# Kernel tuning notes

Hardware: AMD Instinct MI355X
Metric: run time of the kernel (lower is better)

Reference implementation:

```python
import jax, jax.numpy as jnp
import numpy as np

N, D, E = 100000, 32, 1600000
EH, NH = 32, 16
TAU = 0.1


def setup_inputs() -> dict:
    key = jax.random.key(0)
    ks = jax.random.split(key, 12)
    x = jax.random.normal(ks[0], (N, D), dtype=jnp.float32)
    edge_index = jax.random.randint(ks[1], (2, E), 0, N, dtype=jnp.int32)
    hsd = jax.random.normal(ks[2], (N,), dtype=jnp.float32)
    s_e1 = 1.0 / np.sqrt(D + 2)
    s_e2 = 1.0 / np.sqrt(EH)
    s_n2 = 1.0 / np.sqrt(NH)
    We1 = jax.random.uniform(ks[3], (D + 2, EH), jnp.float32, -s_e1, s_e1)
    be1 = jax.random.uniform(ks[4], (EH,), jnp.float32, -s_e1, s_e1)
    We2 = jax.random.uniform(ks[5], (EH, 1), jnp.float32, -s_e2, s_e2)
    be2 = jax.random.uniform(ks[6], (1,), jnp.float32, -s_e2, s_e2)
    Wn1 = jax.random.uniform(ks[7], (1, NH), jnp.float32, -1.0, 1.0)
    bn1 = jax.random.uniform(ks[8], (NH,), jnp.float32, -1.0, 1.0)
    Wn2 = jax.random.uniform(ks[9], (NH, 1), jnp.float32, -s_n2, s_n2)
    bn2 = jax.random.uniform(ks[10], (1,), jnp.float32, -s_n2, s_n2)
    return {"x": x, "hsd": hsd, "We1": We1, "be1": be1, "We2": We2, "be2": be2,
            "Wn1": Wn1, "bn1": bn1, "Wn2": Wn2, "bn2": bn2, "edge_index": edge_index}


def reference(x, hsd, We1, be1, We2, be2, Wn1, bn1, Wn2, bn2, edge_index):
    row, col = edge_index[0], edge_index[1]
    n = x.shape[0]
    # normalized HSD (torch.std is unbiased, ddof=1)
    hsd_norm = (hsd - hsd.mean()) / (jnp.std(hsd, ddof=1) + 1e-8)
    # edge MLP input: [hsd_u, hsd_v, |x_u - x_v|]  -> (E, D+2)
    diff_abs = jnp.abs(x[row] - x[col])
    edge_in = jnp.concatenate([hsd_norm[row][:, None], hsd_norm[col][:, None], diff_abs], axis=1)
    h = jax.nn.relu(edge_in @ We1 + be1)
    e_uv = (h @ We2 + be2)[:, 0]  # (E,)
    # segment softmax over destination (col)
    logits = e_uv / TAU
    seg_max = jax.ops.segment_max(logits, col, num_segments=n)
    seg_max = jnp.where(jnp.isfinite(seg_max), seg_max, 0.0)
    ex = jnp.exp(logits - seg_max[col])
    denom = jax.ops.segment_sum(ex, col, num_segments=n)
    alpha_uv = (ex / (denom[col] + 1e-16))[:, None]  # (E,1)
    # node-level gate
    gh = jax.nn.relu(hsd_norm[:, None] @ Wn1 + bn1)
    alpha_bar = jax.nn.sigmoid(gh @ Wn2 + bn2)  # (N,1)
    # degree normalization
    ones = jnp.ones(row.shape[0], dtype=x.dtype)
    src_deg = jnp.sqrt(jnp.clip(jax.ops.segment_sum(ones, row, num_segments=n), 1.0))
    dst_deg = jnp.sqrt(jnp.clip(jax.ops.segment_sum(ones, col, num_segments=n), 1.0))
    edge_w = 1.0 / (src_deg[row] * dst_deg[col])
    low_pass = jax.ops.segment_sum(edge_w[:, None] * x[row], col, num_segments=n)
    high_pass = jax.ops.segment_sum(alpha_uv * (x[col] - x[row]), col, num_segments=n)
    return (1.0 - alpha_bar) * low_pass + alpha_bar * high_pass
```

## Files before the change

### kernel.cpp

```cpp
#include <hip/hip_runtime.h>

#define D_FEAT 32
#define IN_DIM 34
#define EHID 32
#define NHID 16
#define INV_TAU 10.0f
#define SCAN_CHUNK 1024
#define EPB 256
#define XS 36
#define TILE 8192
#define CAP 7680

__global__ __launch_bounds__(256) void k1_hsd_stats(const float* __restrict__ hsd,
                                                    double* __restrict__ stats, int N) {
    double s = 0.0, s2 = 0.0;
    for (int i = blockIdx.x * 256 + threadIdx.x; i < N; i += gridDim.x * 256) {
        double v = (double)hsd[i];
        s += v; s2 += v * v;
    }
    for (int off = 32; off > 0; off >>= 1) {
        s  += __shfl_down(s,  off, 64);
        s2 += __shfl_down(s2, off, 64);
    }
    __shared__ double ls[4], ls2[4];
    int wid = threadIdx.x >> 6, lid = threadIdx.x & 63;
    if (lid == 0) { ls[wid] = s; ls2[wid] = s2; }
    __syncthreads();
    if (threadIdx.x == 0) {
        double ts = 0.0, t2 = 0.0;
        for (int w = 0; w < 4; ++w) { ts += ls[w]; t2 += ls2[w]; }
        atomicAdd(stats, ts);
        atomicAdd(stats + 1, t2);
    }
}

__global__ __launch_bounds__(256) void k2_node_prep(const float* __restrict__ hsd,
                                                    const double* __restrict__ stats,
                                                    const float* __restrict__ Wn1,
                                                    const float* __restrict__ bn1,
                                                    const float* __restrict__ Wn2,
                                                    const float* __restrict__ bn2,
                                                    float* __restrict__ hsd_norm,
                                                    float* __restrict__ alpha_bar, int N) {
    int n = blockIdx.x * 256 + threadIdx.x;
    if (n >= N) return;
    double sum = stats[0], sumsq = stats[1];
    double mean = sum / (double)N;
    double var  = (sumsq - sum * sum / (double)N) / (double)(N - 1);
    float stdv  = (float)sqrt(var);
    float hn = (hsd[n] - (float)mean) / (stdv + 1e-8f);
    hsd_norm[n] = hn;
    float acc = bn2[0];
#pragma unroll
    for (int k = 0; k < NHID; ++k)
        acc += fmaxf(fmaf(hn, Wn1[k], bn1[k]), 0.0f) * Wn2[k];
    alpha_bar[n] = 1.0f / (1.0f + __expf(-acc));
}

__global__ __launch_bounds__(256) void s1_hist(const int* __restrict__ ei,
                                               int* __restrict__ histV,
                                               int* __restrict__ histU,
                                               int E, int NB, int T) {
    __shared__ int hv[512], hu[512];
    int t = threadIdx.x;
    for (int b = t; b < 512; b += 256) { hv[b] = 0; hu[b] = 0; }
    __syncthreads();
    int base = blockIdx.x * TILE;
    for (int i = t; i < TILE; i += 256) {
        int e = base + i;
        if (e < E) {
            int u = ei[e], v = ei[E + e];
            atomicAdd(&hv[v >> 8], 1);
            atomicAdd(&hu[u >> 8], 1);
        }
    }
    __syncthreads();
    for (int b = t; b < NB; b += 256) {
        histV[b * T + blockIdx.x] = hv[b];
        histU[b * T + blockIdx.x] = hu[b];
    }
}

__global__ __launch_bounds__(256) void scan_k1(const int* __restrict__ cnt,
                                               int* __restrict__ out,
                                               int* __restrict__ partials, int N) {
    __shared__ int lds[256];
    int base = blockIdx.x * SCAN_CHUNK;
    int t = threadIdx.x;
    int v[4]; int loc = 0;
#pragma unroll
    for (int k = 0; k < 4; ++k) {
        int idx = base + t * 4 + k;
        v[k] = (idx < N) ? cnt[idx] : 0;
        loc += v[k];
    }
    lds[t] = loc; __syncthreads();
    for (int off = 1; off < 256; off <<= 1) {
        int a = (t >= off) ? lds[t - off] : 0;
        __syncthreads();
        lds[t] += a;
        __syncthreads();
    }
    int run = (t > 0) ? lds[t - 1] : 0;
    if (t == 255) partials[blockIdx.x] = lds[255];
#pragma unroll
    for (int k = 0; k < 4; ++k) {
        run += v[k];
        int idx = base + t * 4 + k;
        if (idx < N) out[idx + 1] = run;
    }
    if (blockIdx.x == 0 && t == 0) out[0] = 0;
}

__global__ __launch_bounds__(256) void scan_k2(int* __restrict__ partials, int B) {
    __shared__ int lds[256];
    int t = threadIdx.x;
    lds[t] = (t < B) ? partials[t] : 0;
    __syncthreads();
    for (int off = 1; off < 256; off <<= 1) {
        int a = (t >= off) ? lds[t - off] : 0;
        __syncthreads();
        lds[t] += a;
        __syncthreads();
    }
    if (t < B) partials[t] = (t > 0) ? lds[t - 1] : 0;
}

__global__ __launch_bounds__(256) void scan_k3(int* __restrict__ out,
                                               const int* __restrict__ partials, int N) {
    int i = blockIdx.x * 256 + threadIdx.x;
    if (i >= N) return;
    out[i + 1] += partials[i / SCAN_CHUNK];
}

__global__ __launch_bounds__(256) void s2_scatter(const int* __restrict__ ei,
                                                  const int* __restrict__ scanV,
                                                  const int* __restrict__ scanU,
                                                  int2* __restrict__ coarse,
                                                  int* __restrict__ coarseU,
                                                  int E, int NB, int T) {
    __shared__ int curV[512], curU[512];
    int t = threadIdx.x;
    for (int b = t; b < NB; b += 256) {
        curV[b] = scanV[b * T + blockIdx.x];
        curU[b] = scanU[b * T + blockIdx.x];
    }
    __syncthreads();
    int base = blockIdx.x * TILE;
    for (int i = t; i < TILE; i += 256) {
        int e = base + i;
        if (e < E) {
            int u = ei[e], v = ei[E + e];
            int pv = atomicAdd(&curV[v >> 8], 1);
            coarse[pv] = make_int2(u, v);
            int pu = atomicAdd(&curU[u >> 8], 1);
            coarseU[pu] = u;
        }
    }
}

__global__ __launch_bounds__(256) void s3_binsort(int2* __restrict__ coarse,
                                                  const int* __restrict__ scanV,
                                                  int* __restrict__ dst_off,
                                                  int E, int N, int NB, int T) {
    __shared__ int2 buf[CAP];
    __shared__ int cnt[256];
    __shared__ int cur[256];
    int t = threadIdx.x;
    int bin = blockIdx.x;
    int start = scanV[bin * T];
    int endv  = scanV[(bin + 1) * T];
    int n = endv - start;
    if (n > CAP) n = CAP;

    for (int i = t; i < n; i += 256) buf[i] = coarse[start + i];
    cnt[t] = 0;
    __syncthreads();
    for (int i = t; i < n; i += 256) atomicAdd(&cnt[buf[i].y & 255], 1);
    __syncthreads();
    for (int off = 1; off < 256; off <<= 1) {
        int a = (t >= off) ? cnt[t - off] : 0;
        __syncthreads();
        cnt[t] += a;
        __syncthreads();
    }
    int mybase = (t > 0) ? cnt[t - 1] : 0;
    int vglob = (bin << 8) + t;
    if (vglob < N) dst_off[vglob] = start + mybase;
    if (bin == 0 && t == 0) dst_off[N] = E;
    cur[t] = mybase;
    __syncthreads();
    for (int i = t; i < n; i += 256) {
        int lv = buf[i].y & 255;
        int p = atomicAdd(&cur[lv], 1);
        coarse[start + p] = buf[i];
    }
}

__global__ __launch_bounds__(256) void s3b_srccnt(const int* __restrict__ coarseU,
                                                  const int* __restrict__ scanU,
                                                  int* __restrict__ src_cnt,
                                                  int N, int NB, int T) {
    __shared__ int cnt[256];
    int t = threadIdx.x;
    int bin = blockIdx.x;
    int start = scanU[bin * T];
    int endv  = scanU[(bin + 1) * T];
    cnt[t] = 0;
    __syncthreads();
    for (int i = start + t; i < endv; i += 256) atomicAdd(&cnt[coarseU[i] & 255], 1);
    __syncthreads();
    int vglob = (bin << 8) + t;
    if (vglob < N) src_cnt[vglob] = cnt[t];
}

__global__ __launch_bounds__(256) void k3c_mlp(const float* __restrict__ x,
                                               const float* __restrict__ hsd_norm,
                                               const float* __restrict__ We1,
                                               const float* __restrict__ be1,
                                               const float* __restrict__ We2,
                                               const float* __restrict__ be2,
                                               const int2* __restrict__ esorted,
                                               float* __restrict__ logit_sorted, int E) {
    __shared__ float sxu[EPB * XS];
    int t = threadIdx.x;
    int base = blockIdx.x * EPB;

    int q = t & 7;
#pragma unroll
    for (int k = 0; k < 8; ++k) {
        int s = (t >> 3) + 32 * k;
        int e = base + s;
        int u = esorted[(e < E) ? e : (E - 1)].x;
        float4 val = *(const float4*)(x + (size_t)u * D_FEAT + 4 * q);
        *(float4*)(sxu + s * XS + 4 * q) = val;
    }
    __syncthreads();

    int e = base + t;
    if (e >= E) return;
    int2 uv = esorted[e];
    int u = uv.x, v = uv.y;

    float in0 = hsd_norm[u];
    float in1 = hsd_norm[v];

    float diff[D_FEAT];
    const float4* xv = (const float4*)(x + (size_t)v * D_FEAT);
#pragma unroll
    for (int qq = 0; qq < 8; ++qq) {
        float4 a = *(const float4*)(sxu + t * XS + 4 * qq);
        float4 b = xv[qq];
        diff[4 * qq + 0] = fabsf(a.x - b.x);
        diff[4 * qq + 1] = fabsf(a.y - b.y);
        diff[4 * qq + 2] = fabsf(a.z - b.z);
        diff[4 * qq + 3] = fabsf(a.w - b.w);
    }

    float h[EHID];
#pragma unroll
    for (int j = 0; j < EHID; ++j)
        h[j] = fmaf(in0, We1[j], fmaf(in1, We1[EHID + j], be1[j]));
#pragma unroll
    for (int i = 0; i < D_FEAT; ++i) {
        float a = diff[i];
#pragma unroll
        for (int j = 0; j < EHID; ++j)
            h[j] = fmaf(a, We1[(i + 2) * EHID + j], h[j]);
    }
    float acc = be2[0];
#pragma unroll
    for (int j = 0; j < EHID; ++j)
        acc += fmaxf(h[j], 0.0f) * We2[j];

    logit_sorted[e] = acc * INV_TAU;
}

__global__ __launch_bounds__(256) void k5_gather(const float* __restrict__ x,
                                                 const int* __restrict__ dst_off,
                                                 const int2* __restrict__ esorted,
                                                 const float* __restrict__ logit_sorted,
                                                 const int* __restrict__ src_cnt,
                                                 const float* __restrict__ alpha_bar,
                                                 float* __restrict__ out, int N) {
    int wid = threadIdx.x >> 6;
    int lane = threadIdx.x & 63;
    int v = blockIdx.x * 4 + wid;
    if (v >= N) return;

    int beg = dst_off[v], end = dst_off[v + 1];

    float m = -INFINITY;
    for (int t = beg + lane; t < end; t += 64) m = fmaxf(m, logit_sorted[t]);
#pragma unroll
    for (int off = 1; off < 64; off <<= 1) m = fmaxf(m, __shfl_xor(m, off, 64));
    float s = 0.0f;
    for (int t = beg + lane; t < end; t += 64) s += __expf(logit_sorted[t] - m);
#pragma unroll
    for (int off = 1; off < 64; off <<= 1) s += __shfl_xor(s, off, 64);
    float denom = s;
    float inv_denom = 1.0f / (denom + 1e-16f);

    float ab = alpha_bar[v];
    float one_ab = 1.0f - ab;
    float inv_sdv = rsqrtf(fmaxf((float)(end - beg), 1.0f));
    int half = lane >> 5;
    int d = lane & 31;

    float acc = 0.0f;
    int jj = beg + half;
    for (; jj + 2 < end; jj += 4) {
        int u0 = esorted[jj].x;
        int u1 = esorted[jj + 2].x;
        float lg0 = logit_sorted[jj];
        float lg1 = logit_sorted[jj + 2];
        float x0 = x[(size_t)u0 * D_FEAT + d];
        float x1 = x[(size_t)u1 * D_FEAT + d];
        float is0 = rsqrtf(fmaxf((float)src_cnt[u0], 1.0f));
        float is1 = rsqrtf(fmaxf((float)src_cnt[u1], 1.0f));
        float c0 = fmaf(-ab * __expf(lg0 - m), inv_denom, one_ab * is0 * inv_sdv);
        float c1 = fmaf(-ab * __expf(lg1 - m), inv_denom, one_ab * is1 * inv_sdv);
        acc = fmaf(c0, x0, acc);
        acc = fmaf(c1, x1, acc);
    }
    for (; jj < end; jj += 2) {
        int u0 = esorted[jj].x;
        float lg0 = logit_sorted[jj];
        float x0 = x[(size_t)u0 * D_FEAT + d];
        float is0 = rsqrtf(fmaxf((float)src_cnt[u0], 1.0f));
        float c0 = fmaf(-ab * __expf(lg0 - m), inv_denom, one_ab * is0 * inv_sdv);
        acc = fmaf(c0, x0, acc);
    }
    acc += __shfl_xor(acc, 32, 64);

    if (half == 0) {
        float S = denom * inv_denom;
        out[(size_t)v * D_FEAT + d] = fmaf(ab * S, x[(size_t)v * D_FEAT + d], acc);
    }
}

extern "C" void kernel_launch(void* const* d_in, const int* in_sizes, int n_in,
                              void* d_out, int out_size, void* d_ws, size_t ws_size,
                              hipStream_t stream) {
    const float* x    = (const float*)d_in[0];
    const float* hsd  = (const float*)d_in[1];
    const float* We1  = (const float*)d_in[2];
    const float* be1  = (const float*)d_in[3];
    const float* We2  = (const float*)d_in[4];
    const float* be2  = (const float*)d_in[5];
    const float* Wn1  = (const float*)d_in[6];
    const float* bn1  = (const float*)d_in[7];
    const float* Wn2  = (const float*)d_in[8];
    const float* bn2  = (const float*)d_in[9];
    const int*   ei   = (const int*)d_in[10];
    float* out = (float*)d_out;

    const int N = in_sizes[1];
    const int E = in_sizes[10] / 2;
    const int NB = (N + 255) >> 8;
    const int T  = (E + TILE - 1) / TILE;
    const int M  = NB * T;

    char* ws = (char*)d_ws;
    size_t o = 0;
    auto alloc = [&](size_t bytes) { size_t r = o; o += (bytes + 255) & ~(size_t)255; return r; };
    double* stats     = (double*)(ws + alloc(16));
    int*    src_cnt   = (int*)(ws + alloc((size_t)4 * N));
    int*    dst_off   = (int*)(ws + alloc((size_t)4 * (N + 1)));
    float*  hsd_norm  = (float*)(ws + alloc((size_t)4 * N));
    float*  alpha_bar = (float*)(ws + alloc((size_t)4 * N));
    int*    partials  = (int*)(ws + alloc(1024));
    int*    bufA      = (int*)(ws + alloc((size_t)4 * (M + 1)));
    int*    bufB      = (int*)(ws + alloc((size_t)4 * (M + 1)));
    int*    bufC      = (int*)(ws + alloc((size_t)4 * (M + 1)));
    int2*   coarse    = (int2*)(ws + alloc((size_t)8 * E));
    int*    coarseU   = (int*)(ws + alloc((size_t)4 * E));
    float*  logit_sorted = (float*)coarseU;

    hipMemsetAsync(d_ws, 0, 256, stream);

    k1_hsd_stats<<<256, 256, 0, stream>>>(hsd, stats, N);
    k2_node_prep<<<(N + 255) / 256, 256, 0, stream>>>(hsd, stats, Wn1, bn1, Wn2, bn2,
                                                      hsd_norm, alpha_bar, N);

    s1_hist<<<T, 256, 0, stream>>>(ei, bufA, bufC, E, NB, T);

    int Bs = (M + SCAN_CHUNK - 1) / SCAN_CHUNK;
    scan_k1<<<Bs, 256, 0, stream>>>(bufA, bufB, partials, M);
    scan_k2<<<1, 256, 0, stream>>>(partials, Bs);
    scan_k3<<<(M + 255) / 256, 256, 0, stream>>>(bufB, partials, M);
    scan_k1<<<Bs, 256, 0, stream>>>(bufC, bufA, partials, M);
    scan_k2<<<1, 256, 0, stream>>>(partials, Bs);
    scan_k3<<<(M + 255) / 256, 256, 0, stream>>>(bufA, partials, M);

    s2_scatter<<<T, 256, 0, stream>>>(ei, bufB, bufA, coarse, coarseU, E, NB, T);
    s3b_srccnt<<<NB, 256, 0, stream>>>(coarseU, bufA, src_cnt, N, NB, T);
    s3_binsort<<<NB, 256, 0, stream>>>(coarse, bufB, dst_off, E, N, NB, T);

    k3c_mlp<<<(E + EPB - 1) / EPB, 256, 0, stream>>>(x, hsd_norm, We1, be1, We2, be2,
                                                     coarse, logit_sorted, E);
    k5_gather<<<(N + 3) / 4, 256, 0, stream>>>(x, dst_off, coarse, logit_sorted,
                                               src_cnt, alpha_bar, out, N);
}
```

Baseline: 315.4 us.

## Fuse fine bin sort into per-bin gather kernel and merge histogram scans

```diff
diff --git a/kernel.cpp b/kernel.cpp
--- a/kernel.cpp
+++ b/kernel.cpp
@@ -9,7 +9,7 @@
 #define EPB 256
 #define XS 36
 #define TILE 8192
-#define CAP 7680
+#define CAP 6144
 
 __global__ __launch_bounds__(256) void k1_hsd_stats(const float* __restrict__ hsd,
                                                     double* __restrict__ stats, int N) {
@@ -58,9 +58,8 @@
 }
 
 __global__ __launch_bounds__(256) void s1_hist(const int* __restrict__ ei,
-                                               int* __restrict__ histV,
-                                               int* __restrict__ histU,
-                                               int E, int NB, int T) {
+                                               int* __restrict__ hist,
+                                               int E, int NB, int T, int M) {
     __shared__ int hv[512], hu[512];
     int t = threadIdx.x;
     for (int b = t; b < 512; b += 256) { hv[b] = 0; hu[b] = 0; }
@@ -76,8 +75,8 @@
     }
     __syncthreads();
     for (int b = t; b < NB; b += 256) {
-        histV[b * T + blockIdx.x] = hv[b];
-        histU[b * T + blockIdx.x] = hu[b];
+        hist[b * T + blockIdx.x] = hv[b];
+        hist[M + b * T + blockIdx.x] = hu[b];
     }
 }
 
@@ -134,16 +133,15 @@
 }
 
 __global__ __launch_bounds__(256) void s2_scatter(const int* __restrict__ ei,
-                                                  const int* __restrict__ scanV,
-                                                  const int* __restrict__ scanU,
+                                                  const int* __restrict__ scanAll,
                                                   int2* __restrict__ coarse,
                                                   int* __restrict__ coarseU,
-                                                  int E, int NB, int T) {
+                                                  int E, int NB, int T, int M) {
     __shared__ int curV[512], curU[512];
     int t = threadIdx.x;
     for (int b = t; b < NB; b += 256) {
-        curV[b] = scanV[b * T + blockIdx.x];
-        curU[b] = scanU[b * T + blockIdx.x];
+        curV[b] = scanAll[b * T + blockIdx.x];
+        curU[b] = scanAll[M + b * T + blockIdx.x] - E;
     }
     __syncthreads();
     int base = blockIdx.x * TILE;
@@ -159,53 +157,15 @@
     }
 }
 
-__global__ __launch_bounds__(256) void s3_binsort(int2* __restrict__ coarse,
-                                                  const int* __restrict__ scanV,
-                                                  int* __restrict__ dst_off,
-                                                  int E, int N, int NB, int T) {
-    __shared__ int2 buf[CAP];
+__global__ __launch_bounds__(256) void s3b_srccnt(const int* __restrict__ coarseU,
+                                                  const int* __restrict__ scanAll,
+                                                  int* __restrict__ src_cnt,
+                                                  int N, int E, int NB, int T, int M) {
     __shared__ int cnt[256];
-    __shared__ int cur[256];
     int t = threadIdx.x;
     int bin = blockIdx.x;
-    int start = scanV[bin * T];
-    int endv  = scanV[(bin + 1) * T];
-    int n = endv - start;
-    if (n > CAP) n = CAP;
-
-    for (int i = t; i < n; i += 256) buf[i] = coarse[start + i];
-    cnt[t] = 0;
-    __syncthreads();
-    for (int i = t; i < n; i += 256) atomicAdd(&cnt[buf[i].y & 255], 1);
-    __syncthreads();
-    for (int off = 1; off < 256; off <<= 1) {
-        int a = (t >= off) ? cnt[t - off] : 0;
-        __syncthreads();
-        cnt[t] += a;
-        __syncthreads();
-    }
-    int mybase = (t > 0) ? cnt[t - 1] : 0;
-    int vglob = (bin << 8) + t;
-    if (vglob < N) dst_off[vglob] = start + mybase;
-    if (bin == 0 && t == 0) dst_off[N] = E;
-    cur[t] = mybase;
-    __syncthreads();
-    for (int i = t; i < n; i += 256) {
-        int lv = buf[i].y & 255;
-        int p = atomicAdd(&cur[lv], 1);
-        coarse[start + p] = buf[i];
-    }
-}
-
-__global__ __launch_bounds__(256) void s3b_srccnt(const int* __restrict__ coarseU,
-                                                  const int* __restrict__ scanU,
-                                                  int* __restrict__ src_cnt,
-                                                  int N, int NB, int T) {
-    __shared__ int cnt[256];
-    int t = threadIdx.x;
-    int bin = blockIdx.x;
-    int start = scanU[bin * T];
-    int endv  = scanU[(bin + 1) * T];
+    int start = scanAll[M + bin * T] - E;
+    int endv  = scanAll[M + (bin + 1) * T] - E;
     cnt[t] = 0;
     __syncthreads();
     for (int i = start + t; i < endv; i += 256) atomicAdd(&cnt[coarseU[i] & 255], 1);
@@ -221,7 +181,7 @@
                                                const float* __restrict__ We2,
                                                const float* __restrict__ be2,
                                                const int2* __restrict__ esorted,
-                                               float* __restrict__ logit_sorted, int E) {
+                                               float* __restrict__ logit, int E) {
     __shared__ float sxu[EPB * XS];
     int t = threadIdx.x;
     int base = blockIdx.x * EPB;
@@ -273,69 +233,104 @@
     for (int j = 0; j < EHID; ++j)
         acc += fmaxf(h[j], 0.0f) * We2[j];
 
-    logit_sorted[e] = acc * INV_TAU;
-}
-
-__global__ __launch_bounds__(256) void k5_gather(const float* __restrict__ x,
-                                                 const int* __restrict__ dst_off,
-                                                 const int2* __restrict__ esorted,
-                                                 const float* __restrict__ logit_sorted,
-                                                 const int* __restrict__ src_cnt,
-                                                 const float* __restrict__ alpha_bar,
-                                                 float* __restrict__ out, int N) {
-    int wid = threadIdx.x >> 6;
-    int lane = threadIdx.x & 63;
-    int v = blockIdx.x * 4 + wid;
-    if (v >= N) return;
-
-    int beg = dst_off[v], end = dst_off[v + 1];
-
-    float m = -INFINITY;
-    for (int t = beg + lane; t < end; t += 64) m = fmaxf(m, logit_sorted[t]);
-#pragma unroll
-    for (int off = 1; off < 64; off <<= 1) m = fmaxf(m, __shfl_xor(m, off, 64));
-    float s = 0.0f;
-    for (int t = beg + lane; t < end; t += 64) s += __expf(logit_sorted[t] - m);
-#pragma unroll
-    for (int off = 1; off < 64; off <<= 1) s += __shfl_xor(s, off, 64);
-    float denom = s;
-    float inv_denom = 1.0f / (denom + 1e-16f);
-
-    float ab = alpha_bar[v];
-    float one_ab = 1.0f - ab;
-    float inv_sdv = rsqrtf(fmaxf((float)(end - beg), 1.0f));
-    int half = lane >> 5;
-    int d = lane & 31;
-
-    float acc = 0.0f;
-    int jj = beg + half;
-    for (; jj + 2 < end; jj += 4) {
-        int u0 = esorted[jj].x;
-        int u1 = esorted[jj + 2].x;
-        float lg0 = logit_sorted[jj];
-        float lg1 = logit_sorted[jj + 2];
-        float x0 = x[(size_t)u0 * D_FEAT + d];
-        float x1 = x[(size_t)u1 * D_FEAT + d];
-        float is0 = rsqrtf(fmaxf((float)src_cnt[u0], 1.0f));
-        float is1 = rsqrtf(fmaxf((float)src_cnt[u1], 1.0f));
-        float c0 = fmaf(-ab * __expf(lg0 - m), inv_denom, one_ab * is0 * inv_sdv);
-        float c1 = fmaf(-ab * __expf(lg1 - m), inv_denom, one_ab * is1 * inv_sdv);
-        acc = fmaf(c0, x0, acc);
-        acc = fmaf(c1, x1, acc);
-    }
-    for (; jj < end; jj += 2) {
-        int u0 = esorted[jj].x;
-        float lg0 = logit_sorted[jj];
-        float x0 = x[(size_t)u0 * D_FEAT + d];
-        float is0 = rsqrtf(fmaxf((float)src_cnt[u0], 1.0f));
-        float c0 = fmaf(-ab * __expf(lg0 - m), inv_denom, one_ab * is0 * inv_sdv);
-        acc = fmaf(c0, x0, acc);
-    }
-    acc += __shfl_xor(acc, 32, 64);
-
-    if (half == 0) {
-        float S = denom * inv_denom;
-        out[(size_t)v * D_FEAT + d] = fmaf(ab * S, x[(size_t)v * D_FEAT + d], acc);
+    logit[e] = acc * INV_TAU;
+}
+
+__global__ __launch_bounds__(512) void k6_bin(const float* __restrict__ x,
+                                              const int2* __restrict__ coarse,
+                                              const float* __restrict__ logit,
+                                              const int* __restrict__ scanAll,
+                                              const int* __restrict__ src_cnt,
+                                              const float* __restrict__ alpha_bar,
+                                              float* __restrict__ out,
+                                              int N, int E, int NB, int T) {
+    __shared__ int   u_pk[CAP];
+    __shared__ float lg[CAP];
+    __shared__ unsigned short sidx[CAP];
+    __shared__ int cnt[256], base[256], cur[256];
+
+    int t = threadIdx.x;
+    int bin = blockIdx.x;
+    int start = scanAll[bin * T];
+    int n = scanAll[(bin + 1) * T] - start;
+    if (n > CAP) n = CAP;
+
+    if (t < 256) cnt[t] = 0;
+    __syncthreads();
+    for (int i = t; i < n; i += 512) {
+        int2 c = coarse[start + i];
+        int vl = c.y & 255;
+        u_pk[i] = c.x | (vl << 17);
+        lg[i] = logit[start + i];
+        atomicAdd(&cnt[vl], 1);
+    }
+    __syncthreads();
+    for (int off = 1; off < 256; off <<= 1) {
+        int a = 0;
+        if (t < 256 && t >= off) a = cnt[t - off];
+        __syncthreads();
+        if (t < 256) cnt[t] += a;
+        __syncthreads();
+    }
+    if (t < 256) { base[t] = (t > 0) ? cnt[t - 1] : 0; cur[t] = base[t]; }
+    __syncthreads();
+    for (int i = t; i < n; i += 512) {
+        int vl = u_pk[i] >> 17;
+        int p = atomicAdd(&cur[vl], 1);
+        sidx[p] = (unsigned short)i;
+    }
+    __syncthreads();
+
+    int w = t >> 6, lane = t & 63, h = lane >> 5, l = lane & 31;
+    int proc = w * 2 + h;
+    for (int k = proc; k < 256; k += 16) {
+        int vg = (bin << 8) + k;
+        if (vg >= N) continue;
+        int beg = base[k], end = cnt[k];
+        int deg = end - beg;
+        float* orow = out + (size_t)vg * D_FEAT;
+        if (deg == 0) { orow[l] = 0.0f; continue; }
+
+        float m = -INFINITY;
+        for (int i = beg + l; i < end; i += 32) m = fmaxf(m, lg[sidx[i]]);
+#pragma unroll
+        for (int off = 1; off < 32; off <<= 1) m = fmaxf(m, __shfl_xor(m, off, 32));
+        float s = 0.0f;
+        for (int i = beg + l; i < end; i += 32) s += __expf(lg[sidx[i]] - m);
+#pragma unroll
+        for (int off = 1; off < 32; off <<= 1) s += __shfl_xor(s, off, 32);
+        float inv_den = 1.0f / (s + 1e-16f);
+
+        float ab = alpha_bar[vg];
+        float one_ab = 1.0f - ab;
+        float inv_sdv = rsqrtf((float)deg);
+
+        float acc = 0.0f;
+        int i = beg;
+        for (; i + 1 < end; i += 2) {
+            int e0 = sidx[i], e1 = sidx[i + 1];
+            int up0 = u_pk[e0], up1 = u_pk[e1];
+            int u0 = up0 & 0x1FFFF, u1 = up1 & 0x1FFFF;
+            float lg0 = lg[e0], lg1 = lg[e1];
+            float x0 = x[(size_t)u0 * D_FEAT + l];
+            float x1 = x[(size_t)u1 * D_FEAT + l];
+            float is0 = rsqrtf(fmaxf((float)src_cnt[u0], 1.0f));
+            float is1 = rsqrtf(fmaxf((float)src_cnt[u1], 1.0f));
+            float c0 = fmaf(-ab * __expf(lg0 - m), inv_den, one_ab * is0 * inv_sdv);
+            float c1 = fmaf(-ab * __expf(lg1 - m), inv_den, one_ab * is1 * inv_sdv);
+            acc = fmaf(c0, x0, acc);
+            acc = fmaf(c1, x1, acc);
+        }
+        if (i < end) {
+            int e0 = sidx[i];
+            int u0 = u_pk[e0] & 0x1FFFF;
+            float x0 = x[(size_t)u0 * D_FEAT + l];
+            float is0 = rsqrtf(fmaxf((float)src_cnt[u0], 1.0f));
+            float c0 = fmaf(-ab * __expf(lg[e0] - m), inv_den, one_ab * is0 * inv_sdv);
+            acc = fmaf(c0, x0, acc);
+        }
+        float S = s * inv_den;
+        orow[l] = fmaf(ab * S, x[(size_t)vg * D_FEAT + l], acc);
     }
 }
 
@@ -360,22 +355,21 @@
     const int NB = (N + 255) >> 8;
     const int T  = (E + TILE - 1) / TILE;
     const int M  = NB * T;
+    const int M2 = 2 * M;
 
     char* ws = (char*)d_ws;
     size_t o = 0;
     auto alloc = [&](size_t bytes) { size_t r = o; o += (bytes + 255) & ~(size_t)255; return r; };
     double* stats     = (double*)(ws + alloc(16));
     int*    src_cnt   = (int*)(ws + alloc((size_t)4 * N));
-    int*    dst_off   = (int*)(ws + alloc((size_t)4 * (N + 1)));
     float*  hsd_norm  = (float*)(ws + alloc((size_t)4 * N));
     float*  alpha_bar = (float*)(ws + alloc((size_t)4 * N));
     int*    partials  = (int*)(ws + alloc(1024));
-    int*    bufA      = (int*)(ws + alloc((size_t)4 * (M + 1)));
-    int*    bufB      = (int*)(ws + alloc((size_t)4 * (M + 1)));
-    int*    bufC      = (int*)(ws + alloc((size_t)4 * (M + 1)));
+    int*    bufH      = (int*)(ws + alloc((size_t)4 * M2));
+    int*    bufS      = (int*)(ws + alloc((size_t)4 * (M2 + 1)));
     int2*   coarse    = (int2*)(ws + alloc((size_t)8 * E));
     int*    coarseU   = (int*)(ws + alloc((size_t)4 * E));
-    float*  logit_sorted = (float*)coarseU;
+    float*  logit     = (float*)coarseU;
 
     hipMemsetAsync(d_ws, 0, 256, stream);
 
@@ -383,22 +377,17 @@
     k2_node_prep<<<(N + 255) / 256, 256, 0, stream>>>(hsd, stats, Wn1, bn1, Wn2, bn2,
                                                       hsd_norm, alpha_bar, N);
 
-    s1_hist<<<T, 256, 0, stream>>>(ei, bufA, bufC, E, NB, T);
-
-    int Bs = (M + SCAN_CHUNK - 1) / SCAN_CHUNK;
-    scan_k1<<<Bs, 256, 0, stream>>>(bufA, bufB, partials, M);
+    s1_hist<<<T, 256, 0, stream>>>(ei, bufH, E, NB, T, M);
+
+    int Bs = (M2 + SCAN_CHUNK - 1) / SCAN_CHUNK;
+    scan_k1<<<Bs, 256, 0, stream>>>(bufH, bufS, partials, M2);
     scan_k2<<<1, 256, 0, stream>>>(partials, Bs);
-    scan_k3<<<(M + 255) / 256, 256, 0, stream>>>(bufB, partials, M);
-    scan_k1<<<Bs, 256, 0, stream>>>(bufC, bufA, partials, M);
-    scan_k2<<<1, 256, 0, stream>>>(partials, Bs);
-    scan_k3<<<(M + 255) / 256, 256, 0, stream>>>(bufA, partials, M);
-
-    s2_scatter<<<T, 256, 0, stream>>>(ei, bufB, bufA, coarse, coarseU, E, NB, T);
-    s3b_srccnt<<<NB, 256, 0, stream>>>(coarseU, bufA, src_cnt, N, NB, T);
-    s3_binsort<<<NB, 256, 0, stream>>>(coarse, bufB, dst_off, E, N, NB, T);
-
+    scan_k3<<<(M2 + 255) / 256, 256, 0, stream>>>(bufS, partials, M2);
+
+    s2_scatter<<<T, 256, 0, stream>>>(ei, bufS, coarse, coarseU, E, NB, T, M);
+    s3b_srccnt<<<NB, 256, 0, stream>>>(coarseU, bufS, src_cnt, N, E, NB, T, M);
     k3c_mlp<<<(E + EPB - 1) / EPB, 256, 0, stream>>>(x, hsd_norm, We1, be1, We2, be2,
-                                                     coarse, logit_sorted, E);
-    k5_gather<<<(N + 3) / 4, 256, 0, stream>>>(x, dst_off, coarse, logit_sorted,
-                                               src_cnt, alpha_bar, out, N);
-}
+                                                     coarse, logit, E);
+    k6_bin<<<NB, 512, 0, stream>>>(x, coarse, logit, bufS, src_cnt, alpha_bar,
+                                   out, N, E, NB, T);
+}
```

After: 315.8 us. No clear change (+0.1%).
